# Performance work log

Measured on AMD Instinct MI355X. Metric: run time of the kernel, lower is better.

Reference implementation:

```python
import jax, jax.numpy as jnp
import numpy as np
from jax import lax

EPS_BN = 1e-5
EPS_LN = 1e-5
IMG = 240
BETA = 1.0

def l2norm(x, axis=-1):
    n = jnp.linalg.norm(x, axis=axis, keepdims=True)
    return x / jnp.maximum(n, 1e-12)

def bn2d(x, g, b):
    # training-mode BatchNorm2d: stats over (B,H,W), biased variance
    m = x.mean(axis=(0, 2, 3), keepdims=True)
    v = x.var(axis=(0, 2, 3), keepdims=True)
    return g[None, :, None, None] * (x - m) * lax.rsqrt(v + EPS_BN) + b[None, :, None, None]

def conv2d(x, w):
    return lax.conv_general_dilated(x, w, (1, 1), 'SAME', dimension_numbers=('NCHW', 'OIHW', 'NCHW'))

def convT2x2(x, w, b):
    # ConvTranspose2d k=2 s=2 pad=0; torch weight layout (C_in, C_out, 2, 2)
    B, C, H, W = x.shape
    O = w.shape[1]
    y = jnp.einsum('bchw,copq->bohpwq', x, w).reshape(B, O, 2 * H, 2 * W)
    return y + b[None, :, None, None]

def layernorm(x, g, b):
    m = x.mean(-1, keepdims=True)
    v = x.var(-1, keepdims=True)
    return g * (x - m) * lax.rsqrt(v + EPS_LN) + b

def setup_inputs() -> dict:
    key = jax.random.key(0)
    ks = jax.random.split(key, 12)
    L, B, K, N, D = 3, 16, 8, 256, 768
    H, MID = 128, 64
    inp = {
        'query': jax.random.normal(ks[0], (L, B, N, D), jnp.float32),
        'prompt': jax.random.normal(ks[1], (L, B, K, N, D), jnp.float32),
        'sharebn_g': jnp.ones((L, D)), 'sharebn_b': jnp.zeros((L, D)),
        'lw1': 0.02 * jax.random.normal(ks[2], (L, H, D, 3, 3)),
        'lbn1g': jnp.ones((L, H)), 'lbn1b': jnp.zeros((L, H)),
        'lwt1': 0.05 * jax.random.normal(ks[3], (L, H, H, 2, 2)), 'lbt1': jnp.zeros((L, H)),
        'lw2': 0.02 * jax.random.normal(ks[4], (L, MID, H, 3, 3)),
        'lbn2g': jnp.ones((L, MID)), 'lbn2b': jnp.zeros((L, MID)),
        'lwt2': 0.05 * jax.random.normal(ks[5], (L, MID, MID, 2, 2)), 'lbt2': jnp.zeros((L, MID)),
        'lw3': 0.05 * jax.random.normal(ks[6], (L, 2, MID, 1, 1)), 'lb3': jnp.zeros((L, 2)),
        'pool_logits': jnp.zeros((L, 2)),
        'mw1': 0.02 * jax.random.normal(ks[7], (L, H, D)),
        'mlng': jnp.ones((L, H)), 'mlnb': jnp.zeros((L, H)),
        'mw2': 0.05 * jax.random.normal(ks[8], (L, 2, H)), 'mb2': jnp.zeros((L, 2)),
    }
    return inp

def _layer(q, pf, p):
    # q: [B,N,D], pf: [B,M,D]
    B, N, D = q.shape
    g = int(N ** 0.5)
    qn = l2norm(q)
    pn = l2norm(pf)
    sim = jnp.einsum('bnc,bmc->bnm', qn, pn)              # [B,N,M]
    max_cos = sim.max(axis=-1)
    idx = sim.argmax(axis=-1)                              # [B,N]
    aligned = jnp.take_along_axis(pf, idx[:, :, None], axis=1)  # [B,N,D]
    residual = 0.5 * (1.0 - max_cos)
    an = l2norm(aligned)
    ctx = qn + BETA * jnp.abs(qn - an)                     # [B,N,D]
    cmap = ctx.transpose(0, 2, 1).reshape(B, D, g, g)
    cmap = bn2d(cmap, p['sbg'], p['sbb'])
    # local conv head
    x = jax.nn.relu(bn2d(conv2d(cmap, p['w1']), p['bn1g'], p['bn1b']))
    x = convT2x2(x, p['wt1'], p['bt1'])
    x = jax.nn.relu(bn2d(conv2d(x, p['w2']), p['bn2g'], p['bn2b']))
    x = convT2x2(x, p['wt2'], p['bt2'])
    raw = conv2d(x, p['w3']) + p['b3'][None, :, None, None]   # [B,2,4g,4g]
    # adaptive_avg_pool2d 4g -> g (exact 4x4 blocks)
    pl2c = raw.reshape(B, 2, g, 4, g, 4).mean(axis=(3, 5))    # [B,2,g,g]
    ps2c = jax.nn.softmax(pl2c, axis=1)
    patch_logits = (pl2c[:, 1] - pl2c[:, 0]).reshape(B, -1)
    patch_scores = ps2c[:, 1].reshape(B, -1)
    local_logits = jax.image.resize(raw, (B, 2, IMG, IMG), method='bilinear')
    # global head (GAP/GMP fusion over context map features)
    cf = cmap.reshape(B, D, N)
    gap = cf.mean(axis=-1)
    gmp = cf.max(axis=-1)
    pw = jax.nn.softmax(p['pl'])
    pooled = pw[0] * gap + pw[1] * gmp                     # [B,D]
    h = jax.nn.relu(layernorm(pooled @ p['mw1'].T, p['lng'], p['lnb']))
    logits2 = h @ p['mw2'].T + p['mb2']
    glogit = logits2[:, 1] - logits2[:, 0]
    return residual, patch_scores, patch_logits, glogit, local_logits, pw, idx, aligned

def reference(query, prompt, sharebn_g, sharebn_b, lw1, lbn1g, lbn1b, lwt1, lbt1,
              lw2, lbn2g, lbn2b, lwt2, lbt2, lw3, lb3, pool_logits,
              mw1, mlng, mlnb, mw2, mb2):
    L, B = query.shape[0], query.shape[1]
    outs = []
    for l in range(L):
        pf = prompt[l].reshape(B, -1, prompt.shape[-1])
        p = dict(sbg=sharebn_g[l], sbb=sharebn_b[l], w1=lw1[l], bn1g=lbn1g[l], bn1b=lbn1b[l],
                 wt1=lwt1[l], bt1=lbt1[l], w2=lw2[l], bn2g=lbn2g[l], bn2b=lbn2b[l],
                 wt2=lwt2[l], bt2=lbt2[l], w3=lw3[l], b3=lb3[l], pl=pool_logits[l],
                 mw1=mw1[l], lng=mlng[l], lnb=mlnb[l], mw2=mw2[l], mb2=mb2[l])
        outs.append(_layer(query[l], pf, p))
    stacked = tuple(jnp.stack([o[i] for o in outs]) for i in range(8))
    return stacked
```

## Files before the change

kernel.cpp:

```cpp
#include <hip/hip_runtime.h>
#include <hip/hip_bf16.h>
#include <math.h>

#define LLY 3
#define BB 16
#define NNQ 256
#define DD 768
#define MMP 2048
#define HH 128
#define MD 64
#define IMGSZ 240
#define LBTOT (LLY*BB)

#define OFF_INVQ 0
#define OFF_INVP (OFF_INVQ + LLY*BB*NNQ)
#define OFF_CMAP (OFF_INVP + LLY*BB*MMP)
#define OFF_BNSH (OFF_CMAP + LLY*BB*DD*NNQ)
#define OFF_X1   (OFF_BNSH + 2*LLY*DD)
#define OFF_BN1  (OFF_X1 + LLY*BB*HH*256)
#define OFF_T1   (OFF_BN1 + 2*LLY*HH)
#define OFF_X2   (OFF_T1 + LLY*BB*HH*1024)
#define OFF_BN2  (OFF_X2 + LLY*BB*MD*1024)
#define OFF_T2   (OFF_BN2 + 2*LLY*MD)
#define OFF_RAW3 (OFF_T2 + LLY*BB*MD*4096)
#define WS_FLOATS (OFF_RAW3 + LLY*BB*2*4096)
#define T1BSH (LBTOT*1024*HH)
#define SQH   (LBTOT*NNQ*DD)
#define OFF_C1P (OFF_T2 + 4718592)
#define OFF_C2P (OFF_T2 + 3256320)
#define OFF_PGL OFF_X1

#define O_RES 0
#define O_PSC (O_RES + LLY*BB*NNQ)
#define O_PLG (O_PSC + LLY*BB*NNQ)
#define O_GLG (O_PLG + LLY*BB*NNQ)
#define O_LOC (O_GLG + LLY*BB)
#define O_PW  (O_LOC + LLY*BB*2*IMGSZ*IMGSZ)
#define O_IDX (O_PW + LLY*2)
#define O_ALN (O_IDX + LLY*BB*NNQ)

typedef __attribute__((ext_vector_type(8))) short bf16x8;
typedef __attribute__((ext_vector_type(4))) float f32x4;

__device__ __forceinline__ unsigned short f2bf(float f) {
    __hip_bfloat16 h = __float2bfloat16(f);
    unsigned short u;
    __builtin_memcpy(&u, &h, sizeof(u));
    return u;
}
__device__ __forceinline__ float bf2f(unsigned short h) {
    return __uint_as_float(((unsigned int)h) << 16);
}

__device__ __forceinline__ float blockReduceSum(float v, float* sm) {
    for (int o = 32; o; o >>= 1) v += __shfl_down(v, o, 64);
    __syncthreads();
    if ((threadIdx.x & 63) == 0) sm[threadIdx.x >> 6] = v;
    __syncthreads();
    return sm[0] + sm[1] + sm[2] + sm[3];
}

__global__ __launch_bounds__(192) void knormq(const float* __restrict__ query,
                                              float* __restrict__ ws) {
    __shared__ float sm[3];
    int row = blockIdx.x;
    int t = threadIdx.x;
    float4 v = *(const float4*)(query + (size_t)row * DD + t * 4);
    float ss = v.x * v.x + v.y * v.y + v.z * v.z + v.w * v.w;
    for (int o = 32; o; o >>= 1) ss += __shfl_down(ss, o, 64);
    if ((t & 63) == 0) sm[t >> 6] = ss;
    __syncthreads();
    ss = sm[0] + sm[1] + sm[2];
    float iv = 1.0f / fmaxf(sqrtf(ss), 1e-12f);
    if (t == 0) ws[OFF_INVQ + row] = iv;
    unsigned short* qh = (unsigned short*)(ws + OFF_T2);
    unsigned short* ql = qh + SQH;
    float e[4] = {v.x * iv, v.y * iv, v.z * iv, v.w * iv};
    unsigned int hp[2], lp[2];
    #pragma unroll
    for (int j = 0; j < 2; j++) {
        unsigned short h0 = f2bf(e[2*j]), h1 = f2bf(e[2*j+1]);
        unsigned short l0 = f2bf(e[2*j] - bf2f(h0)), l1 = f2bf(e[2*j+1] - bf2f(h1));
        hp[j] = (unsigned int)h0 | ((unsigned int)h1 << 16);
        lp[j] = (unsigned int)l0 | ((unsigned int)l1 << 16);
    }
    *(uint2*)(qh + (size_t)row * DD + t * 4) = make_uint2(hp[0], hp[1]);
    *(uint2*)(ql + (size_t)row * DD + t * 4) = make_uint2(lp[0], lp[1]);
}

__global__ __launch_bounds__(512) void ksimm(const float* __restrict__ prompt, float* __restrict__ ws) {
    __shared__ __align__(16) unsigned short Ah[128][40];
    __shared__ __align__(16) unsigned short Al[128][40];
    __shared__ __align__(16) unsigned short Bh[256][40];
    __shared__ __align__(16) unsigned short Bl[256][40];
    __shared__ float invL[128];
    int bid = blockIdx.x;
    int mt = bid & 15;
    int lb = bid >> 4;
    int t = threadIdx.x;
    int lane = t & 63, wave = t >> 6;
    int wm = wave >> 2, wn = wave & 3;
    int fr = lane & 15, fq = lane >> 4;
    const unsigned short* qh = (const unsigned short*)(ws + OFF_T2);
    const unsigned short* ql = qh + SQH;
    const float* pbase = prompt + (size_t)lb * MMP * DD + (size_t)(mt * 128) * DD;

    float ssq[2] = {0.f, 0.f};

    f32x4 acc[4][4];
    #pragma unroll
    for (int mi = 0; mi < 4; mi++)
        #pragma unroll
        for (int ni = 0; ni < 4; ni++) acc[mi][ni] = (f32x4){0.f, 0.f, 0.f, 0.f};

    for (int kc = 0; kc < DD; kc += 32) {
        __syncthreads();
        #pragma unroll
        for (int i = 0; i < 2; i++) {
            int f = t + i * 512;
            int row = f >> 3, c4 = f & 7;
            float4 v = *(const float4*)(pbase + (size_t)row * DD + kc + c4 * 4);
            ssq[i] += v.x * v.x + v.y * v.y + v.z * v.z + v.w * v.w;
            unsigned short h0 = f2bf(v.x), h1 = f2bf(v.y), h2 = f2bf(v.z), h3 = f2bf(v.w);
            unsigned short l0 = f2bf(v.x - bf2f(h0)), l1 = f2bf(v.y - bf2f(h1));
            unsigned short l2 = f2bf(v.z - bf2f(h2)), l3 = f2bf(v.w - bf2f(h3));
            uint2 hp = make_uint2((unsigned int)h0 | ((unsigned int)h1 << 16),
                                  (unsigned int)h2 | ((unsigned int)h3 << 16));
            uint2 lp = make_uint2((unsigned int)l0 | ((unsigned int)l1 << 16),
                                  (unsigned int)l2 | ((unsigned int)l3 << 16));
            *(uint2*)&Ah[row][c4 * 4] = hp;
            *(uint2*)&Al[row][c4 * 4] = lp;
        }
        #pragma unroll
        for (int i = 0; i < 2; i++) {
            int f = t + i * 512;
            int row = f >> 2, sg = f & 3;
            size_t go = (size_t)(lb * NNQ + row) * DD + kc + sg * 8;
            *(uint4*)&Bh[row][sg * 8] = *(const uint4*)(qh + go);
            *(uint4*)&Bl[row][sg * 8] = *(const uint4*)(ql + go);
        }
        __syncthreads();
        bf16x8 ah[4], al4[4], bh[4], bl4[4];
        #pragma unroll
        for (int mi = 0; mi < 4; mi++) {
            ah[mi]  = *(const bf16x8*)&Ah[wm * 64 + mi * 16 + fr][fq * 8];
            al4[mi] = *(const bf16x8*)&Al[wm * 64 + mi * 16 + fr][fq * 8];
        }
        #pragma unroll
        for (int ni = 0; ni < 4; ni++) {
            bh[ni]  = *(const bf16x8*)&Bh[wn * 64 + ni * 16 + fr][fq * 8];
            bl4[ni] = *(const bf16x8*)&Bl[wn * 64 + ni * 16 + fr][fq * 8];
        }
        #pragma unroll
        for (int mi = 0; mi < 4; mi++)
            #pragma unroll
            for (int ni = 0; ni < 4; ni++) {
                acc[mi][ni] = __builtin_amdgcn_mfma_f32_16x16x32_bf16(ah[mi],  bh[ni],  acc[mi][ni], 0, 0, 0);
                acc[mi][ni] = __builtin_amdgcn_mfma_f32_16x16x32_bf16(ah[mi],  bl4[ni], acc[mi][ni], 0, 0, 0);
                acc[mi][ni] = __builtin_amdgcn_mfma_f32_16x16x32_bf16(al4[mi], bh[ni],  acc[mi][ni], 0, 0, 0);
            }
    }
    #pragma unroll
    for (int i = 0; i < 2; i++) {
        float s = ssq[i];
        s += __shfl_xor(s, 1, 64);
        s += __shfl_xor(s, 2, 64);
        s += __shfl_xor(s, 4, 64);
        if ((t & 7) == 0) {
            int row = (t >> 3) + 64 * i;
            float iv = 1.0f / fmaxf(sqrtf(s), 1e-12f);
            invL[row] = iv;
            ws[OFF_INVP + lb * MMP + mt * 128 + row] = iv;
        }
    }
    __syncthreads();
    float* bestv = ws + OFF_X1;
    float* besti = ws + OFF_X1 + (size_t)LBTOT * NNQ * 32;
    #pragma unroll
    for (int ni = 0; ni < 4; ni++) {
        float bv = -1e30f; int bi = 0;
        #pragma unroll
        for (int mi = 0; mi < 4; mi++)
            #pragma unroll
            for (int rr = 0; rr < 4; rr++) {
                int lm = wm * 64 + mi * 16 + fq * 4 + rr;
                float s = acc[mi][ni][rr] * invL[lm];
                int m = mt * 128 + lm;
                if (s > bv) { bv = s; bi = m; }
            }
        #pragma unroll
        for (int o = 16; o <= 32; o <<= 1) {
            float ov = __shfl_xor(bv, o, 64);
            int oi = __shfl_xor(bi, o, 64);
            if (ov > bv || (ov == bv && oi < bi)) { bv = ov; bi = oi; }
        }
        if (fq == 0) {
            int q = wn * 64 + ni * 16 + fr;
            size_t slot = (size_t)(lb * NNQ + q) * 32 + wm * 16 + mt;
            bestv[slot] = bv;
            besti[slot] = (float)bi;
        }
    }
}

__global__ __launch_bounds__(256) void kpost(const float* __restrict__ query,
                                             const float* __restrict__ prompt,
                                             float* __restrict__ ws,
                                             float* __restrict__ out) {
    __shared__ float red_v[16];
    __shared__ int   red_i[16];
    __shared__ float Lctx[DD * 17];
    int bid = blockIdx.x;
    int nt = bid & 15;
    int lb = bid >> 4;
    int t = threadIdx.x;
    const float* bestv = ws + OFF_X1;
    const float* besti = ws + OFF_X1 + (size_t)LBTOT * NNQ * 32;
    if (t < 16) {
        int q = nt * 16 + t;
        const float* bv = bestv + (size_t)(lb * NNQ + q) * 32;
        const float* bi = besti + (size_t)(lb * NNQ + q) * 32;
        float best = -1e30f; int bidx2 = 0;
        for (int mtt = 0; mtt < 16; mtt++)
            #pragma unroll
            for (int wm = 0; wm < 2; wm++) {
                float v = bv[wm * 16 + mtt];
                if (v > best) { best = v; bidx2 = (int)bi[wm * 16 + mtt]; }
            }
        red_v[t] = best; red_i[t] = bidx2;
        out[O_RES + lb * NNQ + q] = 0.5f * (1.0f - best);
        out[O_IDX + lb * NNQ + q] = (float)bidx2;
    }
    __syncthreads();
    const float* qbase = query + (size_t)(lb * NNQ + nt * 16) * DD;
    const float* pbase = prompt + (size_t)lb * MMP * DD;
    const float* invq = ws + OFF_INVQ + lb * NNQ + nt * 16;
    const float* invp = ws + OFF_INVP + lb * MMP;
    int c = t & 15;
    int nn = t >> 4;
    int gn = nt * 16 + nn;
    int midx = red_i[nn];
    float ip = invp[midx];
    float iq = invq[nn];
    const float* prow = pbase + (size_t)midx * DD;
    const float* qrow = qbase + (size_t)nn * DD;
    float* aln = out + O_ALN + (size_t)(lb * NNQ + gn) * DD;
    for (int jj = 0; jj < DD / 16; jj++) {
        int d = c + jj * 16;
        float pvr = prow[d];
        float qv = qrow[d] * iq;
        float av = pvr * ip;
        float cx = qv + fabsf(qv - av);
        aln[d] = pvr;
        Lctx[d * 17 + nn] = cx;
    }
    __syncthreads();
    float* cm = ws + OFF_CMAP + (size_t)lb * DD * NNQ + nt * 16;
    int nl = t & 15, dd = t >> 4;
    for (int jj = 0; jj < DD / 16; jj++) {
        int d = jj * 16 + dd;
        cm[(size_t)d * NNQ + nl] = Lctx[d * 17 + nl];
    }
}

__global__ __launch_bounds__(256) void kbnstats(const float* __restrict__ x, int C, int SP,
                                                const float* __restrict__ g,
                                                const float* __restrict__ b,
                                                float* __restrict__ outSB) {
    __shared__ float sm[4];
    int bid = blockIdx.x;
    int c = bid % C;
    int l = bid / C;
    int t = threadIdx.x;
    float s = 0.f, sq = 0.f;
    for (int bb2 = 0; bb2 < BB; ++bb2) {
        const float* p = x + ((size_t)(l * BB + bb2) * C + c) * SP;
        for (int i = t; i < SP; i += 256) { float v = p[i]; s += v; sq += v * v; }
    }
    s = blockReduceSum(s, sm);
    sq = blockReduceSum(sq, sm);
    if (t == 0) {
        float inv = 1.0f / (float)(BB * SP);
        float m = s * inv;
        float var = sq * inv - m * m;
        float sc = g[l * C + c] * rsqrtf(var + 1e-5f);
        float bo = b[l * C + c] - m * sc;
        outSB[l * C + c] = sc;
        outSB[LLY * C + l * C + c] = bo;
    }
}

__global__ __launch_bounds__(256) void kw1cvt(const float* __restrict__ lw1, float* __restrict__ ws) {
    unsigned short* w1B = (unsigned short*)(ws + OFF_X2);
    int bid = blockIdx.x;
    int l = bid / HH, co = bid % HH;
    int t = threadIdx.x;
    for (int c0 = 0; c0 < DD; c0 += 256) {
        int ci = c0 + t;
        const float* src = lw1 + ((size_t)(l * HH + co) * DD + ci) * 9;
        #pragma unroll
        for (int tap = 0; tap < 9; tap++) {
            w1B[((size_t)((l * 9 + tap) * HH + co)) * DD + ci] = f2bf(src[tap]);
        }
    }
}

__global__ __launch_bounds__(256) void kbn1cvt(float* __restrict__ ws) {
    __shared__ float Ld[64][65];
    unsigned short* cmT = (unsigned short*)(ws + OFF_T2);
    int bid = blockIdx.x;
    int nt = bid & 3;
    int r = bid >> 2;
    int ct = r % 12;
    int lb = r / 12;
    int l = lb >> 4;
    int t = threadIdx.x;
    const float* cmap = ws + OFF_CMAP + (size_t)lb * DD * NNQ;
    const float* bns = ws + OFF_BNSH + l * DD;
    const float* bnb = ws + OFF_BNSH + LLY * DD + l * DD;
    #pragma unroll
    for (int i = 0; i < 4; i++) {
        int f = t + i * 256;
        int row = f >> 4, c4 = f & 15;
        int ci = ct * 64 + row;
        float4 v = *(const float4*)(cmap + (size_t)ci * NNQ + nt * 64 + c4 * 4);
        float s = bns[ci], bo = bnb[ci];
        Ld[row][c4*4+0] = v.x * s + bo; Ld[row][c4*4+1] = v.y * s + bo;
        Ld[row][c4*4+2] = v.z * s + bo; Ld[row][c4*4+3] = v.w * s + bo;
    }
    __syncthreads();
    #pragma unroll
    for (int i = 0; i < 2; i++) {
        int f = t + i * 256;
        int row = f >> 3, seg = f & 7;
        unsigned int pk[4];
        #pragma unroll
        for (int e = 0; e < 4; e++) {
            unsigned int lo = f2bf(Ld[seg * 8 + 2 * e][row]);
            unsigned int hi = f2bf(Ld[seg * 8 + 2 * e + 1][row]);
            pk[e] = lo | (hi << 16);
        }
        uint4 o = make_uint4(pk[0], pk[1], pk[2], pk[3]);
        *(uint4*)(cmT + ((size_t)(lb * NNQ + nt * 64 + row)) * DD + ct * 64 + seg * 8) = o;
    }
}

__global__ __launch_bounds__(256) void kconv1m(float* __restrict__ ws) {
    __shared__ __align__(16) unsigned short Ab[128][72];
    __shared__ __align__(16) unsigned short Bb[128][72];
    int bid = blockIdx.x;
    int s = bid % 6;
    int ntile = (bid / 6) & 1;
    int lb = bid / 12;
    int l = lb >> 4;
    int t = threadIdx.x;
    int lane = t & 63;
    int wave = t >> 6;
    int wr = wave >> 1, wc = wave & 1;
    int fr = lane & 15, fq = lane >> 4;
    const unsigned short* w1B = (const unsigned short*)(ws + OFF_X2);
    const unsigned short* cmT = (const unsigned short*)(ws + OFF_T2);

    f32x4 acc[4][4];
    #pragma unroll
    for (int mi = 0; mi < 4; mi++)
        #pragma unroll
        for (int ni = 0; ni < 4; ni++) acc[mi][ni] = (f32x4){0.f, 0.f, 0.f, 0.f};

    for (int g = s * 18; g < s * 18 + 18; ++g) {
        int tap = g / 12;
        int kc = (g % 12) * 64;
        int dy = tap / 3 - 1, dx = tap % 3 - 1;
        const unsigned short* wpl = w1B + (size_t)((l * 9 + tap) * HH) * DD;
        __syncthreads();
        #pragma unroll
        for (int i = 0; i < 4; i++) {
            int f = t + i * 256;
            int row = f >> 3, seg = f & 7;
            uint4 v = *(const uint4*)(wpl + (size_t)row * DD + kc + seg * 8);
            *(uint4*)&Ab[row][seg * 8] = v;
        }
        #pragma unroll
        for (int i = 0; i < 4; i++) {
            int f = t + i * 256;
            int row = f >> 3, seg = f & 7;
            int n = ntile * 128 + row;
            int y = (n >> 4) + dy, x = (n & 15) + dx;
            bool ok = ((unsigned)y < 16u) && ((unsigned)x < 16u);
            uint4 v = make_uint4(0u, 0u, 0u, 0u);
            if (ok) v = *(const uint4*)(cmT + ((size_t)(lb * NNQ + y * 16 + x)) * DD + kc + seg * 8);
            *(uint4*)&Bb[row][seg * 8] = v;
        }
        __syncthreads();
        #pragma unroll
        for (int kk = 0; kk < 64; kk += 32) {
            bf16x8 af[4], bfv[4];
            #pragma unroll
            for (int mi = 0; mi < 4; mi++)
                af[mi] = *(const bf16x8*)&Ab[wr * 64 + mi * 16 + fr][kk + fq * 8];
            #pragma unroll
            for (int ni = 0; ni < 4; ni++)
                bfv[ni] = *(const bf16x8*)&Bb[wc * 64 + ni * 16 + fr][kk + fq * 8];
            #pragma unroll
            for (int mi = 0; mi < 4; mi++)
                #pragma unroll
                for (int ni = 0; ni < 4; ni++)
                    acc[mi][ni] = __builtin_amdgcn_mfma_f32_16x16x32_bf16(af[mi], bfv[ni], acc[mi][ni], 0, 0, 0);
        }
    }
    float* dst = (s == 5) ? (ws + OFF_X1 + (size_t)lb * HH * 256)
                          : (ws + OFF_C1P + (size_t)(s * LBTOT + lb) * (HH * 256));
    #pragma unroll
    for (int mi = 0; mi < 4; mi++) {
        #pragma unroll
        for (int ni = 0; ni < 4; ni++) {
            int gn = ntile * 128 + wc * 64 + ni * 16 + fr;
            #pragma unroll
            for (int rr = 0; rr < 4; rr++) {
                int co = wr * 64 + mi * 16 + fq * 4 + rr;
                dst[(size_t)co * 256 + gn] = acc[mi][ni][rr];
            }
        }
    }
}

__global__ __launch_bounds__(256) void kc1red(float* __restrict__ ws) {
    size_t i = ((size_t)blockIdx.x * 256 + threadIdx.x) * 8;
    float4 a0 = *(float4*)(ws + OFF_X1 + i);
    float4 a1 = *(float4*)(ws + OFF_X1 + i + 4);
    #pragma unroll
    for (int s = 0; s < 5; s++) {
        const float* p = ws + OFF_C1P + (size_t)s * (LBTOT * HH * 256) + i;
        float4 b0 = *(const float4*)p;
        float4 b1 = *(const float4*)(p + 4);
        a0.x += b0.x; a0.y += b0.y; a0.z += b0.z; a0.w += b0.w;
        a1.x += b1.x; a1.y += b1.y; a1.z += b1.z; a1.w += b1.w;
    }
    *(float4*)(ws + OFF_X1 + i) = a0;
    *(float4*)(ws + OFF_X1 + i + 4) = a1;
}

__global__ __launch_bounds__(256) void kconvT(const float* __restrict__ wt,
                                              const float* __restrict__ bt,
                                              const float* __restrict__ xin,
                                              const float* __restrict__ sbsb,
                                              float* __restrict__ xout,
                                              int CI, int CO, int gsh, int nTiles, int oTiles) {
    __shared__ __align__(16) float In[16][256];
    __shared__ __align__(16) float Wc[16][32];
    int bid = blockIdx.x;
    int ntile = bid % nTiles;
    int rem = bid / nTiles;
    int pq = rem & 3; rem >>= 2;
    int ot = rem % oTiles;
    int lb = rem / oTiles;
    int l = lb >> 4;
    int SPIN = 1 << (2 * gsh);
    int t = threadIdx.x, tc = t >> 5, tn = t & 31;
    const float* sc = sbsb + l * CI;
    const float* bo = sbsb + LLY * CI + l * CI;
    float acc[4][8] = {};

    for (int cc = 0; cc < CI; cc += 16) {
        __syncthreads();
        #pragma unroll
        for (int i = 0; i < 4; i++) {
            int fid = t + i * 256;
            int r = fid >> 6, c4 = fid & 63;
            int ci = cc + r;
            float4 v = *(const float4*)(xin + (size_t)(lb * CI + ci) * SPIN + ntile * 256 + c4 * 4);
            float s = sc[ci], bb_ = bo[ci];
            v.x = fmaxf(v.x * s + bb_, 0.f); v.y = fmaxf(v.y * s + bb_, 0.f);
            v.z = fmaxf(v.z * s + bb_, 0.f); v.w = fmaxf(v.w * s + bb_, 0.f);
            *(float4*)&In[r][c4 * 4] = v;
        }
        #pragma unroll
        for (int i = 0; i < 2; i++) {
            int idx = t + i * 256;
            int c_l = idx >> 5, o_l = idx & 31;
            Wc[c_l][o_l] = wt[((size_t)(l * CI + cc + c_l) * CO + ot * 32 + o_l) * 4 + pq];
        }
        __syncthreads();
        #pragma unroll
        for (int ci = 0; ci < 16; ci++) {
            float4 w4 = *(const float4*)&Wc[ci][tc * 4];
            #pragma unroll
            for (int j = 0; j < 8; j++) {
                float in = In[ci][tn + 32 * j];
                acc[0][j] += w4.x * in;
                acc[1][j] += w4.y * in;
                acc[2][j] += w4.z * in;
                acc[3][j] += w4.w * in;
            }
        }
    }
    int p = pq >> 1, q = pq & 1;
    int GIN = 1 << gsh;
    #pragma unroll
    for (int q2 = 0; q2 < 4; q2++) {
        int o = ot * 32 + tc * 4 + q2;
        float bias = bt[l * CO + o];
        float* orow = xout + (size_t)(lb * CO + o) * (4 * SPIN);
        #pragma unroll
        for (int j = 0; j < 8; j++) {
            int n = ntile * 256 + tn + 32 * j;
            int h = n >> gsh, w = n & (GIN - 1);
            orow[(2 * h + p) * (2 * GIN) + 2 * w + q] = acc[q2][j] + bias;
        }
    }
}

__global__ __launch_bounds__(256) void kt1cvt(float* __restrict__ ws) {
    __shared__ float Ld[64][65];
    unsigned short* t1B = (unsigned short*)(ws + OFF_T2);
    int bid = blockIdx.x;
    int ntile = bid & 15;
    int r = bid >> 4;
    int ct = r & 1;
    int lb = r >> 1;
    int t = threadIdx.x;
    const float* t1p = ws + OFF_T1 + (size_t)lb * HH * 1024;
    #pragma unroll
    for (int i = 0; i < 4; i++) {
        int f = t + i * 256;
        int row = f >> 4, c4 = f & 15;
        float4 v = *(const float4*)(t1p + (size_t)(ct * 64 + row) * 1024 + ntile * 64 + c4 * 4);
        *(float4*)&Ld[row][c4 * 4] = v;
    }
    __syncthreads();
    #pragma unroll
    for (int i = 0; i < 2; i++) {
        int f = t + i * 256;
        int row = f >> 3, seg = f & 7;
        unsigned int pk[4];
        #pragma unroll
        for (int e = 0; e < 4; e++) {
            unsigned int lo = f2bf(Ld[seg * 8 + 2 * e][row]);
            unsigned int hi = f2bf(Ld[seg * 8 + 2 * e + 1][row]);
            pk[e] = lo | (hi << 16);
        }
        uint4 o = make_uint4(pk[0], pk[1], pk[2], pk[3]);
        *(uint4*)(t1B + ((size_t)(lb * 1024 + ntile * 64 + row)) * HH + ct * 64 + seg * 8) = o;
    }
}

__global__ __launch_bounds__(256) void kw2cvt(const float* __restrict__ lw2, float* __restrict__ ws) {
    unsigned short* w2B = (unsigned short*)(ws + OFF_T2) + T1BSH;
    int bid = blockIdx.x;
    int l = bid / MD, co = bid % MD;
    int t = threadIdx.x;
    if (t < HH) {
        int ci = t;
        const float* src = lw2 + ((size_t)(l * MD + co) * HH + ci) * 9;
        #pragma unroll
        for (int tap = 0; tap < 9; tap++) {
            w2B[((size_t)((l * 9 + tap) * MD + co)) * HH + ci] = f2bf(src[tap]);
        }
    }
}

__global__ __launch_bounds__(256) void kconv2m(float* __restrict__ ws) {
    __shared__ __align__(16) unsigned short Ab[64][72];
    __shared__ __align__(16) unsigned short Bb[256][72];
    int bid = blockIdx.x;
    int s = bid & 1;
    int ntile = (bid >> 1) & 3;
    int lb = bid >> 3;
    int l = lb >> 4;
    int t = threadIdx.x;
    int lane = t & 63;
    int wave = t >> 6;
    int fr = lane & 15, fq = lane >> 4;
    const unsigned short* t1B = (const unsigned short*)(ws + OFF_T2);
    const unsigned short* w2B = (const unsigned short*)(ws + OFF_T2) + T1BSH;

    f32x4 acc[4][4];
    #pragma unroll
    for (int mi = 0; mi < 4; mi++)
        #pragma unroll
        for (int ni = 0; ni < 4; ni++) acc[mi][ni] = (f32x4){0.f, 0.f, 0.f, 0.f};

    for (int g = s * 9; g < s * 9 + 9; ++g) {
        int tap = g >> 1;
        int kc = (g & 1) * 64;
        int dy = tap / 3 - 1, dx = tap % 3 - 1;
        const unsigned short* wpl = w2B + (size_t)((l * 9 + tap) * MD) * HH;
        __syncthreads();
        #pragma unroll
        for (int i = 0; i < 2; i++) {
            int f = t + i * 256;
            int row = f >> 3, seg = f & 7;
            uint4 v = *(const uint4*)(wpl + (size_t)row * HH + kc + seg * 8);
            *(uint4*)&Ab[row][seg * 8] = v;
        }
        #pragma unroll
        for (int i = 0; i < 8; i++) {
            int f = t + i * 256;
            int row = f >> 3, seg = f & 7;
            int n = ntile * 256 + row;
            int y = (n >> 5) + dy, x = (n & 31) + dx;
            bool ok = ((unsigned)y < 32u) && ((unsigned)x < 32u);
            uint4 v = make_uint4(0u, 0u, 0u, 0u);
            if (ok) v = *(const uint4*)(t1B + ((size_t)(lb * 1024 + y * 32 + x)) * HH + kc + seg * 8);
            *(uint4*)&Bb[row][seg * 8] = v;
        }
        __syncthreads();
        #pragma unroll
        for (int kk = 0; kk < 64; kk += 32) {
            bf16x8 af[4], bfv[4];
            #pragma unroll
            for (int mi = 0; mi < 4; mi++)
                af[mi] = *(const bf16x8*)&Ab[mi * 16 + fr][kk + fq * 8];
            #pragma unroll
            for (int ni = 0; ni < 4; ni++)
                bfv[ni] = *(const bf16x8*)&Bb[wave * 64 + ni * 16 + fr][kk + fq * 8];
            #pragma unroll
            for (int mi = 0; mi < 4; mi++)
                #pragma unroll
                for (int ni = 0; ni < 4; ni++)
                    acc[mi][ni] = __builtin_amdgcn_mfma_f32_16x16x32_bf16(af[mi], bfv[ni], acc[mi][ni], 0, 0, 0);
        }
    }
    float* dst = (s == 1) ? (ws + OFF_X2 + (size_t)lb * MD * 1024)
                          : (ws + OFF_C2P + (size_t)lb * MD * 1024);
    #pragma unroll
    for (int mi = 0; mi < 4; mi++) {
        #pragma unroll
        for (int ni = 0; ni < 4; ni++) {
            int gn = ntile * 256 + wave * 64 + ni * 16 + fr;
            #pragma unroll
            for (int rr = 0; rr < 4; rr++) {
                int co = mi * 16 + fq * 4 + rr;
                dst[(size_t)co * 1024 + gn] = acc[mi][ni][rr];
            }
        }
    }
}

__global__ __launch_bounds__(256) void kc2red(float* __restrict__ ws) {
    size_t i = ((size_t)blockIdx.x * 256 + threadIdx.x) * 8;
    float4 a0 = *(float4*)(ws + OFF_X2 + i);
    float4 a1 = *(float4*)(ws + OFF_X2 + i + 4);
    const float* p = ws + OFF_C2P + i;
    float4 b0 = *(const float4*)p;
    float4 b1 = *(const float4*)(p + 4);
    a0.x += b0.x; a0.y += b0.y; a0.z += b0.z; a0.w += b0.w;
    a1.x += b1.x; a1.y += b1.y; a1.z += b1.z; a1.w += b1.w;
    *(float4*)(ws + OFF_X2 + i) = a0;
    *(float4*)(ws + OFF_X2 + i + 4) = a1;
}

__global__ __launch_bounds__(256) void kconv3(const float* __restrict__ lw3,
                                              const float* __restrict__ lb3,
                                              float* __restrict__ ws) {
    __shared__ float w3s[2][64];
    int bid = blockIdx.x;
    int tile = bid & 15;
    int lb = bid >> 4;
    int l = lb >> 4;
    int t = threadIdx.x;
    if (t < 128) w3s[t >> 6][t & 63] = lw3[(size_t)(l * 2 + (t >> 6)) * MD + (t & 63)];
    __syncthreads();
    const float* t2p = ws + OFF_T2 + (size_t)lb * MD * 4096;
    int hw = tile * 256 + t;
    float a0 = lb3[l * 2], a1 = lb3[l * 2 + 1];
    for (int c2 = 0; c2 < MD; c2++) {
        float v = t2p[(size_t)c2 * 4096 + hw];
        a0 += v * w3s[0][c2];
        a1 += v * w3s[1][c2];
    }
    float* r3 = ws + OFF_RAW3 + (size_t)lb * 2 * 4096;
    r3[hw] = a0;
    r3[4096 + hw] = a1;
}

__global__ __launch_bounds__(256) void kpool(const float* __restrict__ ws, float* __restrict__ out) {
    int lb = blockIdx.x;
    int t = threadIdx.x;
    int gy = t >> 4, gx = t & 15;
    const float* r3 = ws + OFF_RAW3 + (size_t)lb * 2 * 4096;
    float pl[2];
    #pragma unroll
    for (int ch = 0; ch < 2; ch++) {
        const float* basep = r3 + ch * 4096;
        float s = 0.f;
        #pragma unroll
        for (int dy = 0; dy < 4; dy++)
            #pragma unroll
            for (int dx = 0; dx < 4; dx++)
                s += basep[(gy * 4 + dy) * 64 + gx * 4 + dx];
        pl[ch] = s * (1.f / 16.f);
    }
    out[O_PLG + lb * NNQ + t] = pl[1] - pl[0];
    out[O_PSC + lb * NNQ + t] = 1.f / (1.f + expf(pl[0] - pl[1]));
}

__global__ __launch_bounds__(256) void kresize(const float* __restrict__ ws, float* __restrict__ out) {
    int id = blockIdx.x * 256 + threadIdx.x;
    int ox = id % IMGSZ;
    int tmp = id / IMGSZ;
    int oy = tmp % IMGSZ;
    int tmp2 = tmp / IMGSZ;
    int ch = tmp2 & 1;
    int lb = tmp2 >> 1;
    const float S = 64.f / 240.f;
    float xs = fminf(fmaxf((ox + 0.5f) * S - 0.5f, 0.f), 63.f);
    float ys = fminf(fmaxf((oy + 0.5f) * S - 0.5f, 0.f), 63.f);
    int x0 = (int)xs, y0 = (int)ys;
    float fx = xs - x0, fy = ys - y0;
    int x1 = min(x0 + 1, 63), y1 = min(y0 + 1, 63);
    const float* basep = ws + OFF_RAW3 + (size_t)(lb * 2 + ch) * 4096;
    float v00 = basep[y0 * 64 + x0], v01 = basep[y0 * 64 + x1];
    float v10 = basep[y1 * 64 + x0], v11 = basep[y1 * 64 + x1];
    float v = (1.f - fy) * ((1.f - fx) * v00 + fx * v01) + fy * ((1.f - fx) * v10 + fx * v11);
    out[O_LOC + id] = v;
}

__global__ __launch_bounds__(256) void kgap(float* __restrict__ ws,
                                            const float* __restrict__ pool_logits) {
    int bid = blockIdx.x;
    int dchunk = bid % 12;
    int lb = bid / 12;
    int l = lb >> 4;
    int t = threadIdx.x;
    int r = t >> 2, p = t & 3;
    int d = dchunk * 64 + r;
    const float* row = ws + OFF_CMAP + (size_t)lb * DD * NNQ + (size_t)d * NNQ + p * 64;
    float s = 0.f, mx = -1e30f, mn = 1e30f;
    #pragma unroll
    for (int i = 0; i < 16; i++) {
        float4 v = *(const float4*)(row + i * 4);
        s += v.x + v.y + v.z + v.w;
        mx = fmaxf(mx, fmaxf(fmaxf(v.x, v.y), fmaxf(v.z, v.w)));
        mn = fminf(mn, fminf(fminf(v.x, v.y), fminf(v.z, v.w)));
    }
    s += __shfl_xor(s, 1, 64); s += __shfl_xor(s, 2, 64);
    mx = fmaxf(mx, __shfl_xor(mx, 1, 64)); mx = fmaxf(mx, __shfl_xor(mx, 2, 64));
    mn = fminf(mn, __shfl_xor(mn, 1, 64)); mn = fminf(mn, __shfl_xor(mn, 2, 64));
    if (p == 0) {
        float p0 = pool_logits[l * 2], p1 = pool_logits[l * 2 + 1];
        float mxp = fmaxf(p0, p1);
        float e0 = expf(p0 - mxp), e1 = expf(p1 - mxp);
        float pw0 = e0 / (e0 + e1), pw1 = e1 / (e0 + e1);
        const float* bns = ws + OFF_BNSH + l * DD;
        const float* bnb = ws + OFF_BNSH + LLY * DD + l * DD;
        float scv = bns[d], bov = bnb[d];
        float gap = scv * (s * (1.f / NNQ)) + bov;
        float gmp = (scv >= 0.f) ? (scv * mx + bov) : (scv * mn + bov);
        ws[OFF_PGL + lb * DD + d] = pw0 * gap + pw1 * gmp;
    }
}

__global__ __launch_bounds__(256) void kglob2(const float* __restrict__ ws,
                                              const float* __restrict__ pool_logits,
                                              const float* __restrict__ mw1,
                                              const float* __restrict__ mlng,
                                              const float* __restrict__ mlnb,
                                              const float* __restrict__ mw2,
                                              const float* __restrict__ mb2,
                                              float* __restrict__ out) {
    __shared__ float pooled[DD];
    __shared__ float zbuf[HH];
    __shared__ float hbuf[HH];
    __shared__ float sm[4];
    int lb = blockIdx.x;
    int l = lb >> 4;
    int b = lb & 15;
    int t = threadIdx.x;
    float p0 = pool_logits[l * 2], p1 = pool_logits[l * 2 + 1];
    float mx = fmaxf(p0, p1);
    float e0 = expf(p0 - mx), e1 = expf(p1 - mx);
    float pw0 = e0 / (e0 + e1), pw1 = e1 / (e0 + e1);
    if (b == 0 && t < 2) out[O_PW + l * 2 + t] = (t == 0) ? pw0 : pw1;

    for (int d = t; d < DD; d += 256) pooled[d] = ws[OFF_PGL + lb * DD + d];
    __syncthreads();
    if (t < HH) {
        const float* wrow = mw1 + (size_t)(l * HH + t) * DD;
        float a = 0.f;
        for (int d2 = 0; d2 < DD; d2++) a += pooled[d2] * wrow[d2];
        zbuf[t] = a;
    }
    __syncthreads();
    float zv = (t < HH) ? zbuf[t] : 0.f;
    float s1r = blockReduceSum(zv, sm);
    float s2r = blockReduceSum(zv * zv, sm);
    float mean = s1r * (1.f / HH);
    float var = s2r * (1.f / HH) - mean * mean;
    float rstd = rsqrtf(var + 1e-5f);
    if (t < HH) {
        float h = (zbuf[t] - mean) * rstd * mlng[l * HH + t] + mlnb[l * HH + t];
        hbuf[t] = fmaxf(h, 0.f);
    }
    __syncthreads();
    float hv = (t < HH) ? hbuf[t] : 0.f;
    float w0v = (t < HH) ? mw2[(size_t)(l * 2 + 0) * HH + t] : 0.f;
    float w1v = (t < HH) ? mw2[(size_t)(l * 2 + 1) * HH + t] : 0.f;
    float s0 = blockReduceSum(hv * w0v, sm);
    float s1 = blockReduceSum(hv * w1v, sm);
    if (t == 0) out[O_GLG + lb] = (s1 + mb2[l * 2 + 1]) - (s0 + mb2[l * 2]);
}

extern "C" void kernel_launch(void* const* d_in, const int* in_sizes, int n_in,
                              void* d_out, int out_size, void* d_ws, size_t ws_size,
                              hipStream_t stream) {
    const float* query      = (const float*)d_in[0];
    const float* prompt     = (const float*)d_in[1];
    const float* sharebn_g  = (const float*)d_in[2];
    const float* sharebn_b  = (const float*)d_in[3];
    const float* lw1        = (const float*)d_in[4];
    const float* lbn1g      = (const float*)d_in[5];
    const float* lbn1b      = (const float*)d_in[6];
    const float* lwt1       = (const float*)d_in[7];
    const float* lbt1       = (const float*)d_in[8];
    const float* lw2        = (const float*)d_in[9];
    const float* lbn2g      = (const float*)d_in[10];
    const float* lbn2b      = (const float*)d_in[11];
    const float* lwt2       = (const float*)d_in[12];
    const float* lbt2       = (const float*)d_in[13];
    const float* lw3        = (const float*)d_in[14];
    const float* lb3        = (const float*)d_in[15];
    const float* pool_logits= (const float*)d_in[16];
    const float* mw1        = (const float*)d_in[17];
    const float* mlng       = (const float*)d_in[18];
    const float* mlnb       = (const float*)d_in[19];
    const float* mw2        = (const float*)d_in[20];
    const float* mb2        = (const float*)d_in[21];
    float* out = (float*)d_out;
    float* ws = (float*)d_ws;

    hipLaunchKernelGGL(knormq, dim3(LLY*BB*NNQ), dim3(192), 0, stream, query, ws);
    hipLaunchKernelGGL(ksimm, dim3(LBTOT*16), dim3(512), 0, stream, prompt, ws);
    hipLaunchKernelGGL(kpost, dim3(LBTOT*16), dim3(256), 0, stream, query, prompt, ws, out);
    hipLaunchKernelGGL(kbnstats, dim3(LLY*DD), dim3(256), 0, stream,
                       ws + OFF_CMAP, DD, NNQ, sharebn_g, sharebn_b, ws + OFF_BNSH);
    hipLaunchKernelGGL(kw1cvt, dim3(LLY*HH), dim3(256), 0, stream, lw1, ws);
    hipLaunchKernelGGL(kbn1cvt, dim3(LBTOT*48), dim3(256), 0, stream, ws);
    hipLaunchKernelGGL(kconv1m, dim3(LBTOT*12), dim3(256), 0, stream, ws);
    hipLaunchKernelGGL(kc1red, dim3(768), dim3(256), 0, stream, ws);
    hipLaunchKernelGGL(kbnstats, dim3(LLY*HH), dim3(256), 0, stream,
                       ws + OFF_X1, HH, 256, lbn1g, lbn1b, ws + OFF_BN1);
    hipLaunchKernelGGL(kconvT, dim3(LBTOT*16), dim3(256), 0, stream,
                       lwt1, lbt1, ws + OFF_X1, ws + OFF_BN1, ws + OFF_T1, HH, HH, 4, 1, 4);
    hipLaunchKernelGGL(kt1cvt, dim3(LBTOT*32), dim3(256), 0, stream, ws);
    hipLaunchKernelGGL(kw2cvt, dim3(LLY*MD), dim3(256), 0, stream, lw2, ws);
    hipLaunchKernelGGL(kconv2m, dim3(LBTOT*8), dim3(256), 0, stream, ws);
    hipLaunchKernelGGL(kc2red, dim3(1536), dim3(256), 0, stream, ws);
    hipLaunchKernelGGL(kbnstats, dim3(LLY*MD), dim3(256), 0, stream,
                       ws + OFF_X2, MD, 1024, lbn2g, lbn2b, ws + OFF_BN2);
    hipLaunchKernelGGL(kconvT, dim3(LBTOT*32), dim3(256), 0, stream,
                       lwt2, lbt2, ws + OFF_X2, ws + OFF_BN2, ws + OFF_T2, MD, MD, 5, 4, 2);
    hipLaunchKernelGGL(kconv3, dim3(LBTOT*16), dim3(256), 0, stream, lw3, lb3, ws);
    hipLaunchKernelGGL(kpool, dim3(LBTOT), dim3(256), 0, stream, ws, out);
    hipLaunchKernelGGL(kresize, dim3(LLY*BB*2*IMGSZ*IMGSZ/256), dim3(256), 0, stream, ws, out);
    hipLaunchKernelGGL(kgap, dim3(LBTOT*12), dim3(256), 0, stream, ws, pool_logits);
    hipLaunchKernelGGL(kglob2, dim3(LBTOT), dim3(256), 0, stream,
                       ws, pool_logits, mw1, mlng, mlnb, mw2, mb2, out);
}
```

Measured before the change: 530.8 us.

## Run transposed convolutions as bf16 MFMA GEMMs with pre-converted operands

Replaces the scalar fp32 transposed-convolution kernel with an MFMA-based kernel using bf16 16x16x32 matrix instructions. New pre-pass kernels apply the batch-norm affine and ReLU, transpose the activations to channel-contiguous bf16, and repack the transposed-conv weights per output-phase into bf16. The intent is to move the two upsampling GEMMs off the fp32 vector ALUs. In exchange it adds extra launches and workspace traffic, aliases scratch regions, and lowers the precision of the activations and weights to bf16.

```diff
diff --git a/kernel.cpp b/kernel.cpp
--- a/kernel.cpp
+++ b/kernel.cpp
@@ -29,6 +29,8 @@
 #define OFF_C1P (OFF_T2 + 4718592)
 #define OFF_C2P (OFF_T2 + 3256320)
 #define OFF_PGL OFF_X1
+#define X1B_SH 0
+#define WT1B_SH 1600000
 
 #define O_RES 0
 #define O_PSC (O_RES + LLY*BB*NNQ)
@@ -440,72 +442,137 @@
     *(float4*)(ws + OFF_X1 + i + 4) = a1;
 }
 
-__global__ __launch_bounds__(256) void kconvT(const float* __restrict__ wt,
-                                              const float* __restrict__ bt,
-                                              const float* __restrict__ xin,
-                                              const float* __restrict__ sbsb,
-                                              float* __restrict__ xout,
-                                              int CI, int CO, int gsh, int nTiles, int oTiles) {
-    __shared__ __align__(16) float In[16][256];
-    __shared__ __align__(16) float Wc[16][32];
+__global__ __launch_bounds__(256) void kxcvt(const float* __restrict__ x,
+                                             const float* __restrict__ sbsb,
+                                             unsigned short* __restrict__ xb,
+                                             int CI, int SPIN, int nT, int cT) {
+    __shared__ float Ld[64][65];
+    int bid = blockIdx.x;
+    int nt = bid % nT;
+    int r = bid / nT;
+    int ct = r % cT;
+    int lb = r / cT;
+    int l = lb >> 4;
+    int t = threadIdx.x;
+    const float* sc = sbsb + l * CI;
+    const float* bo = sbsb + LLY * CI + l * CI;
+    #pragma unroll
+    for (int i = 0; i < 4; i++) {
+        int f = t + i * 256;
+        int row = f >> 4, c4 = f & 15;
+        int ci = ct * 64 + row;
+        float4 v = *(const float4*)(x + ((size_t)lb * CI + ci) * SPIN + nt * 64 + c4 * 4);
+        float s = sc[ci], b_ = bo[ci];
+        Ld[row][c4*4+0] = fmaxf(v.x * s + b_, 0.f);
+        Ld[row][c4*4+1] = fmaxf(v.y * s + b_, 0.f);
+        Ld[row][c4*4+2] = fmaxf(v.z * s + b_, 0.f);
+        Ld[row][c4*4+3] = fmaxf(v.w * s + b_, 0.f);
+    }
+    __syncthreads();
+    int segs = CI >> 3;
+    for (int f = t; f < 64 * segs; f += 256) {
+        int row = f / segs, seg = f % segs;
+        int sl = seg - ct * 8;
+        if (sl < 0 || sl >= 8) continue;
+        unsigned int pk[4];
+        #pragma unroll
+        for (int e = 0; e < 4; e++) {
+            unsigned int lo = f2bf(Ld[sl * 8 + 2 * e][row]);
+            unsigned int hi = f2bf(Ld[sl * 8 + 2 * e + 1][row]);
+            pk[e] = lo | (hi << 16);
+        }
+        uint4 o = make_uint4(pk[0], pk[1], pk[2], pk[3]);
+        *(uint4*)(xb + ((size_t)lb * SPIN + nt * 64 + row) * CI + ct * 64 + sl * 8) = o;
+    }
+}
+
+__global__ __launch_bounds__(128) void kwtcvt(const float* __restrict__ lwt,
+                                              unsigned short* __restrict__ dst,
+                                              int CI, int CO) {
+    int bid = blockIdx.x;
+    int l = bid / CO, co = bid % CO;
+    int t = threadIdx.x;
+    if (t < CI) {
+        const float* src = lwt + (((size_t)(l * CI + t) * CO + co) * 4);
+        #pragma unroll
+        for (int pq = 0; pq < 4; pq++) {
+            dst[((size_t)((l * 4 + pq) * CO + co)) * CI + t] = f2bf(src[pq]);
+        }
+    }
+}
+
+__global__ __launch_bounds__(256) void kconvTm(const unsigned short* __restrict__ xb,
+                                               const unsigned short* __restrict__ wtb,
+                                               const float* __restrict__ bt,
+                                               float* __restrict__ xout,
+                                               int CI, int CO, int gsh, int nTiles, int coTiles) {
+    __shared__ __align__(16) unsigned short Ab[64][72];
+    __shared__ __align__(16) unsigned short Bb[256][72];
     int bid = blockIdx.x;
     int ntile = bid % nTiles;
-    int rem = bid / nTiles;
-    int pq = rem & 3; rem >>= 2;
-    int ot = rem % oTiles;
-    int lb = rem / oTiles;
+    int r = bid / nTiles;
+    int cot = r % coTiles; r /= coTiles;
+    int pq = r & 3;
+    int lb = r >> 2;
     int l = lb >> 4;
     int SPIN = 1 << (2 * gsh);
-    int t = threadIdx.x, tc = t >> 5, tn = t & 31;
-    const float* sc = sbsb + l * CI;
-    const float* bo = sbsb + LLY * CI + l * CI;
-    float acc[4][8] = {};
-
-    for (int cc = 0; cc < CI; cc += 16) {
+    int t = threadIdx.x, lane = t & 63, wave = t >> 6;
+    int fr = lane & 15, fq = lane >> 4;
+
+    f32x4 acc[4][4];
+    #pragma unroll
+    for (int mi = 0; mi < 4; mi++)
+        #pragma unroll
+        for (int ni = 0; ni < 4; ni++) acc[mi][ni] = (f32x4){0.f, 0.f, 0.f, 0.f};
+
+    for (int kc = 0; kc < CI; kc += 64) {
         __syncthreads();
         #pragma unroll
-        for (int i = 0; i < 4; i++) {
-            int fid = t + i * 256;
-            int r = fid >> 6, c4 = fid & 63;
-            int ci = cc + r;
-            float4 v = *(const float4*)(xin + (size_t)(lb * CI + ci) * SPIN + ntile * 256 + c4 * 4);
-            float s = sc[ci], bb_ = bo[ci];
-            v.x = fmaxf(v.x * s + bb_, 0.f); v.y = fmaxf(v.y * s + bb_, 0.f);
-            v.z = fmaxf(v.z * s + bb_, 0.f); v.w = fmaxf(v.w * s + bb_, 0.f);
-            *(float4*)&In[r][c4 * 4] = v;
-        }
-        #pragma unroll
         for (int i = 0; i < 2; i++) {
-            int idx = t + i * 256;
-            int c_l = idx >> 5, o_l = idx & 31;
-            Wc[c_l][o_l] = wt[((size_t)(l * CI + cc + c_l) * CO + ot * 32 + o_l) * 4 + pq];
+            int f = t + i * 256;
+            int row = f >> 3, seg = f & 7;
+            *(uint4*)&Ab[row][seg * 8] =
+                *(const uint4*)(wtb + ((size_t)((l * 4 + pq) * CO + cot * 64 + row)) * CI + kc + seg * 8);
+        }
+        #pragma unroll
+        for (int i = 0; i < 8; i++) {
+            int f = t + i * 256;
+            int row = f >> 3, seg = f & 7;
+            *(uint4*)&Bb[row][seg * 8] =
+                *(const uint4*)(xb + ((size_t)lb * SPIN + ntile * 256 + row) * CI + kc + seg * 8);
         }
         __syncthreads();
         #pragma unroll
-        for (int ci = 0; ci < 16; ci++) {
-            float4 w4 = *(const float4*)&Wc[ci][tc * 4];
-            #pragma unroll
-            for (int j = 0; j < 8; j++) {
-                float in = In[ci][tn + 32 * j];
-                acc[0][j] += w4.x * in;
-                acc[1][j] += w4.y * in;
-                acc[2][j] += w4.z * in;
-                acc[3][j] += w4.w * in;
-            }
+        for (int kk = 0; kk < 64; kk += 32) {
+            bf16x8 af[4], bfv[4];
+            #pragma unroll
+            for (int mi = 0; mi < 4; mi++)
+                af[mi] = *(const bf16x8*)&Ab[mi * 16 + fr][kk + fq * 8];
+            #pragma unroll
+            for (int ni = 0; ni < 4; ni++)
+                bfv[ni] = *(const bf16x8*)&Bb[wave * 64 + ni * 16 + fr][kk + fq * 8];
+            #pragma unroll
+            for (int mi = 0; mi < 4; mi++)
+                #pragma unroll
+                for (int ni = 0; ni < 4; ni++)
+                    acc[mi][ni] = __builtin_amdgcn_mfma_f32_16x16x32_bf16(af[mi], bfv[ni], acc[mi][ni], 0, 0, 0);
         }
     }
     int p = pq >> 1, q = pq & 1;
     int GIN = 1 << gsh;
     #pragma unroll
-    for (int q2 = 0; q2 < 4; q2++) {
-        int o = ot * 32 + tc * 4 + q2;
-        float bias = bt[l * CO + o];
-        float* orow = xout + (size_t)(lb * CO + o) * (4 * SPIN);
-        #pragma unroll
-        for (int j = 0; j < 8; j++) {
-            int n = ntile * 256 + tn + 32 * j;
-            int h = n >> gsh, w = n & (GIN - 1);
-            orow[(2 * h + p) * (2 * GIN) + 2 * w + q] = acc[q2][j] + bias;
+    for (int mi = 0; mi < 4; mi++) {
+        #pragma unroll
+        for (int rr = 0; rr < 4; rr++) {
+            int co = cot * 64 + mi * 16 + fq * 4 + rr;
+            float bias = bt[l * CO + co];
+            float* orow = xout + ((size_t)(lb * CO + co)) * (4 * SPIN);
+            #pragma unroll
+            for (int ni = 0; ni < 4; ni++) {
+                int n = ntile * 256 + wave * 64 + ni * 16 + fr;
+                int h = n >> gsh, w = n & (GIN - 1);
+                orow[(2 * h + p) * (2 * GIN) + 2 * w + q] = acc[mi][ni][rr] + bias;
+            }
         }
     }
 }
@@ -840,16 +907,30 @@
     hipLaunchKernelGGL(kc1red, dim3(768), dim3(256), 0, stream, ws);
     hipLaunchKernelGGL(kbnstats, dim3(LLY*HH), dim3(256), 0, stream,
                        ws + OFF_X1, HH, 256, lbn1g, lbn1b, ws + OFF_BN1);
-    hipLaunchKernelGGL(kconvT, dim3(LBTOT*16), dim3(256), 0, stream,
-                       lwt1, lbt1, ws + OFF_X1, ws + OFF_BN1, ws + OFF_T1, HH, HH, 4, 1, 4);
+    hipLaunchKernelGGL(kxcvt, dim3(LBTOT*8), dim3(256), 0, stream,
+                       ws + OFF_X1, ws + OFF_BN1, (unsigned short*)(ws + OFF_T2) + X1B_SH,
+                       HH, 256, 4, 2);
+    hipLaunchKernelGGL(kwtcvt, dim3(LLY*HH), dim3(128), 0, stream,
+                       lwt1, (unsigned short*)(ws + OFF_T2) + WT1B_SH, HH, HH);
+    hipLaunchKernelGGL(kconvTm, dim3(LBTOT*4*2), dim3(256), 0, stream,
+                       (const unsigned short*)(ws + OFF_T2) + X1B_SH,
+                       (const unsigned short*)(ws + OFF_T2) + WT1B_SH,
+                       lbt1, ws + OFF_T1, HH, HH, 4, 1, 2);
     hipLaunchKernelGGL(kt1cvt, dim3(LBTOT*32), dim3(256), 0, stream, ws);
     hipLaunchKernelGGL(kw2cvt, dim3(LLY*MD), dim3(256), 0, stream, lw2, ws);
     hipLaunchKernelGGL(kconv2m, dim3(LBTOT*8), dim3(256), 0, stream, ws);
     hipLaunchKernelGGL(kc2red, dim3(1536), dim3(256), 0, stream, ws);
     hipLaunchKernelGGL(kbnstats, dim3(LLY*MD), dim3(256), 0, stream,
                        ws + OFF_X2, MD, 1024, lbn2g, lbn2b, ws + OFF_BN2);
-    hipLaunchKernelGGL(kconvT, dim3(LBTOT*32), dim3(256), 0, stream,
-                       lwt2, lbt2, ws + OFF_X2, ws + OFF_BN2, ws + OFF_T2, MD, MD, 5, 4, 2);
+    hipLaunchKernelGGL(kxcvt, dim3(LBTOT*16), dim3(256), 0, stream,
+                       ws + OFF_X2, ws + OFF_BN2, (unsigned short*)(ws + OFF_X1),
+                       MD, 1024, 16, 1);
+    hipLaunchKernelGGL(kwtcvt, dim3(LLY*MD), dim3(128), 0, stream,
+                       lwt2, (unsigned short*)(ws + OFF_X2), MD, MD);
+    hipLaunchKernelGGL(kconvTm, dim3(LBTOT*4*4), dim3(256), 0, stream,
+                       (const unsigned short*)(ws + OFF_X1),
+                       (const unsigned short*)(ws + OFF_X2),
+                       lbt2, ws + OFF_T2, MD, MD, 5, 4, 1);
     hipLaunchKernelGGL(kconv3, dim3(LBTOT*16), dim3(256), 0, stream, lw3, lb3, ws);
     hipLaunchKernelGGL(kpool, dim3(LBTOT), dim3(256), 0, stream, ws, out);
     hipLaunchKernelGGL(kresize, dim3(LLY*BB*2*IMGSZ*IMGSZ/256), dim3(256), 0, stream, ws, out);
```

Result: faster. 516.6 us (-2.7%).
